# Performance work log

Hardware: AMD Instinct MI355X
Metric: run time of the kernel (lower is better)

Reference implementation:

```python
import jax, jax.numpy as jnp
import numpy as np

D = 1024  # model_dim; d_ff == model_dim in this module
EPS = 1e-6

def setup_inputs() -> dict:
    key = jax.random.key(0)
    ks = jax.random.split(key, 8)
    s = 1.0 / np.sqrt(D)
    sg = 1.0 / np.sqrt(2 * D)
    return {
        "x": jax.random.normal(ks[0], (8, 2048, D), dtype=jnp.float32),
        "w1": jax.random.uniform(ks[1], (D, D), jnp.float32, -s, s),
        "b1": jnp.zeros((D,), jnp.float32),
        "w2": jax.random.uniform(ks[2], (D, D), jnp.float32, -s, s),
        "b2": jnp.zeros((D,), jnp.float32),
        "ln_g": jnp.ones((D,), jnp.float32),
        "ln_b": jnp.zeros((D,), jnp.float32),
        "wg": jax.random.uniform(ks[3], (2 * D, 2 * D), jnp.float32, -sg, sg),
        "bg": jnp.zeros((2 * D,), jnp.float32),
    }

def _layernorm(x, g, b):
    mu = jnp.mean(x, axis=-1, keepdims=True)
    var = jnp.mean(jnp.square(x - mu), axis=-1, keepdims=True)
    return (x - mu) * jax.lax.rsqrt(var + EPS) * g + b

def reference(x, w1, b1, w2, b2, ln_g, ln_b, wg, bg):
    B, S, d = x.shape
    # cumulative average: tril-normalized mask matmul == prefix-sum / position
    denom = jnp.arange(1, S + 1, dtype=x.dtype)[:, None]  # [S,1]
    avg = jnp.cumsum(x, axis=1) / denom                    # [B,S,D]
    # PositionwiseFeedForward (dropout is identity at inference)
    inter = jax.nn.relu(_layernorm(avg, ln_g, ln_b) @ w1 + b1)
    avg_out = inter @ w2 + b2 + avg
    # gating
    gates = jnp.concatenate([x, avg_out], axis=-1) @ wg + bg  # [B,S,2D]
    in_g, fg_g = jnp.split(gates, 2, axis=-1)
    gated = jax.nn.sigmoid(in_g) * x + jax.nn.sigmoid(fg_g) * avg_out
    return gated, avg_out
```

## Files before the change

kernel.cpp:

```cpp
#include <hip/hip_runtime.h>

typedef unsigned short u16;
typedef __attribute__((ext_vector_type(8))) short short8;
typedef __attribute__((ext_vector_type(8))) unsigned short ushort8;
typedef __attribute__((ext_vector_type(4))) float f32x4;
typedef __attribute__((ext_vector_type(4))) unsigned short u16x4;

#define DEV static __device__ __forceinline__

DEV u16 f2bf(float f){
    unsigned u = __float_as_uint(f);
    u += 0x7fffu + ((u >> 16) & 1u);
    return (u16)(u >> 16);
}
DEV float bf2f(u16 h){ return __uint_as_float(((unsigned)h) << 16); }
DEV float sigm(float v){ return 1.f / (1.f + __expf(-v)); }

DEV f32x4 MF(short8 a, short8 b, f32x4 c){
    return __builtin_amdgcn_mfma_f32_16x16x32_bf16(a, b, c, 0, 0, 0);
}
DEV void gload16(const void* g, u16* l){
    __builtin_amdgcn_global_load_lds(
        (const __attribute__((address_space(1))) void*)g,
        (__attribute__((address_space(3))) void*)l, 16, 0, 0);
}
DEV void stage_half(const char* gp, size_t K2, u16* dst){
    gload16(gp, dst);
    gload16(gp + (K2 << 3), dst + 512);
}

#define SBAR()   asm volatile("s_barrier" ::: "memory")
#define WVM(n)   asm volatile("s_waitcnt vmcnt(" #n ")" ::: "memory")
#define WLG(n)   asm volatile("s_waitcnt lgkmcnt(" #n ")" ::: "memory")
#define SCB()    __builtin_amdgcn_sched_barrier(0)

constexpr int Bn = 8, Sn = 2048, Dn = 1024;
constexpr int CH = 128, NC = Sn / CH;
constexpr size_t NTOK = (size_t)Bn * Sn;

__global__ __launch_bounds__(256) void k_wcvt(const float* __restrict__ w,
                                              u16* __restrict__ wt,
                                              int Kd, int Nd)
{
    __shared__ float tile[32][33];
    int nbn = Nd / 32;
    int bk = blockIdx.x / nbn, bn = blockIdx.x % nbn;
    int lx = threadIdx.x & 31, ly = threadIdx.x >> 5;
    #pragma unroll
    for (int i = 0; i < 32; i += 8)
        tile[ly + i][lx] = w[(size_t)(bk * 32 + ly + i) * Nd + bn * 32 + lx];
    __syncthreads();
    #pragma unroll
    for (int i = 0; i < 32; i += 8)
        wt[(size_t)(bn * 32 + ly + i) * Kd + bk * 32 + lx] = f2bf(tile[lx][ly + i]);
}

__global__ __launch_bounds__(256) void k_psum(const float* __restrict__ x,
                                              float* __restrict__ part)
{
    int bx = blockIdx.x;
    int dblk = bx & 3; bx >>= 2;
    int c = bx & (NC - 1), b = bx >> 4;
    int d = dblk * 256 + threadIdx.x;
    const float* px = x + ((size_t)b * Sn + (size_t)c * CH) * Dn + d;
    float s = 0.f;
    #pragma unroll 4
    for (int i = 0; i < CH; i++) s += px[(size_t)i * Dn];
    part[((size_t)b * NC + c) * Dn + d] = s;
}

__global__ __launch_bounds__(256) void k_pscan(float* part)
{
    int g = blockIdx.x * 256 + threadIdx.x;
    int b = g >> 10, d = g & 1023;
    float run = 0.f;
    #pragma unroll
    for (int c = 0; c < NC; c++){
        size_t idx = ((size_t)b * NC + c) * Dn + d;
        float v = part[idx]; part[idx] = run; run += v;
    }
}

__global__ __launch_bounds__(256) void k_avg(const float* __restrict__ x,
                                             const float* __restrict__ part,
                                             u16* __restrict__ avg,
                                             u16* __restrict__ cat)
{
    int bx = blockIdx.x;
    int dblk = bx & 3; bx >>= 2;
    int c = bx & (NC - 1), b = bx >> 4;
    int d = dblk * 256 + threadIdx.x;
    const float* px = x   + ((size_t)b * Sn + (size_t)c * CH) * Dn + d;
    u16*         pa = avg + ((size_t)b * Sn + (size_t)c * CH) * Dn + d;
    u16*         pc = cat + ((size_t)b * Sn + (size_t)c * CH) * 2048 + d;
    float run = part[((size_t)b * NC + c) * Dn + d];
    for (int i = 0; i < CH; i++){
        float v = px[(size_t)i * Dn];
        run += v;
        int s = c * CH + i;
        pa[(size_t)i * Dn] = f2bf(run / (float)(s + 1));
        pc[(size_t)i * 2048] = f2bf(v);
    }
}

__global__ __launch_bounds__(256) void k_ln(const u16* __restrict__ avg,
                                            const float* __restrict__ g,
                                            const float* __restrict__ bta,
                                            u16* __restrict__ out)
{
    size_t row = blockIdx.x;
    int t = threadIdx.x;
    u16x4 hv = ((const u16x4*)(avg + row * Dn))[t];
    float4 v = { bf2f(hv[0]), bf2f(hv[1]), bf2f(hv[2]), bf2f(hv[3]) };
    float s = v.x + v.y + v.z + v.w;
    float q = v.x * v.x + v.y * v.y + v.z * v.z + v.w * v.w;
    #pragma unroll
    for (int o = 32; o > 0; o >>= 1){
        s += __shfl_down(s, o, 64);
        q += __shfl_down(q, o, 64);
    }
    __shared__ float rs[4], rq[4];
    __shared__ float smu, srstd;
    int wid = t >> 6, lane = t & 63;
    if (lane == 0){ rs[wid] = s; rq[wid] = q; }
    __syncthreads();
    if (t == 0){
        float S = rs[0] + rs[1] + rs[2] + rs[3];
        float Q = rq[0] + rq[1] + rq[2] + rq[3];
        float mu = S * (1.f / Dn);
        float var = Q * (1.f / Dn) - mu * mu;
        smu = mu; srstd = rsqrtf(var + 1e-6f);
    }
    __syncthreads();
    float mu = smu, rstd = srstd;
    int d0 = t * 4;
    float4 gg = ((const float4*)g)[t];
    float4 bb = ((const float4*)bta)[t];
    u16x4 o;
    o[0] = f2bf((v.x - mu) * rstd * gg.x + bb.x);
    o[1] = f2bf((v.y - mu) * rstd * gg.y + bb.y);
    o[2] = f2bf((v.z - mu) * rstd * gg.z + bb.z);
    o[3] = f2bf((v.w - mu) * rstd * gg.w + bb.w);
    *(u16x4*)(out + row * Dn + d0) = o;
}

template<int EPI>
__global__ __launch_bounds__(512, 2)
void k_gemm(const u16* __restrict__ A, const u16* __restrict__ Bt,
            const float* __restrict__ bias,
            float* __restrict__ of, u16* __restrict__ ob,
            const u16* __restrict__ resid,
            int M, int N, int K)
{
    __shared__ u16 smem[2][2][2][8192];

    int nbn = (EPI == 3) ? 8 : (N >> 8);
    int nwg = (M >> 8) * nbn;
    int bid = blockIdx.x;
    int swz = (bid & 7) * (nwg >> 3) + (bid >> 3);
    int bm = swz / nbn, bn = swz - bm * nbn;
    int m0 = bm << 8;
    int n0 = (EPI == 3) ? (bn << 7) : (bn << 8);

    int tid  = threadIdx.x;
    int wid  = tid >> 6, lane = tid & 63;
    int wm   = wid >> 2, wn = wid & 3;
    int fr   = lane & 15, q = lane >> 4;

    int srow = (wid << 4) + (lane >> 3);
    int cb   = ((lane & 7) << 4) ^ (((lane >> 3) & 7) << 4);
    size_t K2 = (size_t)K * 2;
    int b1base = (EPI == 3) ? (1024 + n0) : (n0 + 128);
    const char* gA0 = (const char*)A  + (size_t)(m0 + srow) * K2 + cb;
    const char* gA1 = (const char*)A  + (size_t)(m0 + 128 + srow) * K2 + cb;
    const char* gB0 = (const char*)Bt + (size_t)(n0 + srow) * K2 + cb;
    const char* gB1 = (const char*)Bt + (size_t)(b1base + srow) * K2 + cb;
    int w16 = wid << 10;

    int xorE = (lane & 7) << 3;
    int cbE0 = ((q << 3) ^ xorE);
    int cbE1 = cbE0 ^ 32;
    int aOff = (wm * 64 + fr) * 64;
    int bOff = (wn * 32 + fr) * 64;

    f32x4 acc[8][4] = {};
    short8 a0f[4][2], a1f[4][2], b0f[2][2], b1f[2][2];
    int NT = K >> 6;

#define ST_A0(t) stage_half(gA0 + (size_t)(t) * 128, K2, &smem[(t)&1][0][0][w16])
#define ST_A1(t) stage_half(gA1 + (size_t)(t) * 128, K2, &smem[(t)&1][0][1][w16])
#define ST_B0(t) stage_half(gB0 + (size_t)(t) * 128, K2, &smem[(t)&1][1][0][w16])
#define ST_B1(t) stage_half(gB1 + (size_t)(t) * 128, K2, &smem[(t)&1][1][1][w16])
#define RD_A(Fr, t, half) { const u16* _p = &smem[(t)&1][0][half][0];           \
    _Pragma("unroll") for (int i = 0; i < 4; i++){                              \
        Fr[i][0] = *(const short8*)&_p[aOff + i * 1024 + cbE0];                 \
        Fr[i][1] = *(const short8*)&_p[aOff + i * 1024 + cbE1]; } }
#define RD_B(Fr, t, half) { const u16* _p = &smem[(t)&1][1][half][0];           \
    _Pragma("unroll") for (int i = 0; i < 2; i++){                              \
        Fr[i][0] = *(const short8*)&_p[bOff + i * 1024 + cbE0];                 \
        Fr[i][1] = *(const short8*)&_p[bOff + i * 1024 + cbE1]; } }
#define MMQ(Af, Bf, mo, no)                                                     \
    __builtin_amdgcn_s_setprio(1);                                              \
    _Pragma("unroll") for (int mi = 0; mi < 4; mi++)                            \
        _Pragma("unroll") for (int ni = 0; ni < 2; ni++){                       \
            acc[mi+(mo)][ni+(no)] = MF(Af[mi][0], Bf[ni][0], acc[mi+(mo)][ni+(no)]); \
            acc[mi+(mo)][ni+(no)] = MF(Af[mi][1], Bf[ni][1], acc[mi+(mo)][ni+(no)]); \
        }                                                                        \
    __builtin_amdgcn_s_setprio(0);

    ST_A0(0); ST_B0(0); ST_B1(0); ST_A1(0); ST_A0(1); ST_B0(1); ST_B1(1);
    WVM(12); SBAR();
    RD_A(a0f, 0, 0);

    for (int t = 0; t + 2 < NT; ++t){
        WVM(8); SBAR();
        ST_A1(t + 1);
        RD_B(b0f, t, 0); SCB();
        RD_B(b1f, t, 1);
        WLG(4); SCB();
        MMQ(a0f, b0f, 0, 0);
        WVM(8); SBAR();
        ST_A0(t + 2);
        RD_A(a1f, t, 1);
        WLG(8); SCB();
        MMQ(a0f, b1f, 0, 2);
        SBAR();
        ST_B0(t + 2);
        WLG(0); SCB();
        MMQ(a1f, b1f, 4, 2);
        WVM(10); SBAR();
        ST_B1(t + 2);
        RD_A(a0f, t + 1, 0);
        WLG(8); SCB();
        MMQ(a1f, b0f, 4, 0);
    }
    {
        int t = NT - 2;
        WVM(8); SBAR();
        ST_A1(t + 1);
        RD_B(b0f, t, 0); SCB();
        RD_B(b1f, t, 1);
        WLG(4); SCB();
        MMQ(a0f, b0f, 0, 0);
        WVM(8); SBAR();
        RD_A(a1f, t, 1);
        WLG(8); SCB();
        MMQ(a0f, b1f, 0, 2);
        SBAR();
        WLG(0); SCB();
        MMQ(a1f, b1f, 4, 2);
        WVM(6); SBAR();
        RD_A(a0f, t + 1, 0);
        WLG(8); SCB();
        MMQ(a1f, b0f, 4, 0);
    }
    {
        int t = NT - 1;
        WVM(2); SBAR();
        RD_B(b0f, t, 0); SCB();
        RD_B(b1f, t, 1);
        WLG(4); SCB();
        MMQ(a0f, b0f, 0, 0);
        WVM(0); SBAR();
        RD_A(a1f, t, 1);
        WLG(8); SCB();
        MMQ(a0f, b1f, 0, 2);
        SBAR();
        WLG(0); SCB();
        MMQ(a1f, b1f, 4, 2);
        MMQ(a1f, b0f, 4, 0);
    }

    int col = lane & 15, rb = q * 4;

    if constexpr (EPI == 3){
        u16* s_in = &smem[0][0][0][0];
        u16* s_fg = s_in + 32768;
        float bi[2], bf_[2];
        #pragma unroll
        for (int ni = 0; ni < 2; ni++){
            bi[ni]  = bias[n0 + wn * 32 + ni * 16 + col];
            bf_[ni] = bias[1024 + n0 + wn * 32 + ni * 16 + col];
        }
        SBAR();
        #pragma unroll
        for (int mi = 0; mi < 8; mi++){
            int lrow = ((mi & 4) << 5) + wm * 64 + ((mi & 3) << 4) + rb;
            #pragma unroll
            for (int ni = 0; ni < 2; ni++){
                int c  = wn * 32 + ni * 16 + col;
                int cp = c ^ (q << 4);
                #pragma unroll
                for (int r = 0; r < 4; r++){
                    int row = lrow + r;
                    s_in[row * 128 + cp] = f2bf(sigm(acc[mi][ni][r] + bi[ni]));
                    s_fg[row * 128 + cp] = f2bf(sigm(acc[mi][ni + 2][r] + bf_[ni]));
                }
            }
        }
        WLG(0); SBAR();
        int rbase = wid * 32;
        #pragma unroll
        for (int rg = 0; rg < 8; rg++){
            int b4  = rbase + rg * 4;
            int row = b4 + (lane >> 4);
            int sw  = ((b4 >> 2) & 3) << 4;
            int c0  = (lane & 15) * 8;
            int cp  = c0 ^ sw;
            ushort8 iv = *(const ushort8*)&s_in[row * 128 + cp];
            ushort8 fv = *(const ushort8*)&s_fg[row * 128 + cp];
            size_t ga = (size_t)(m0 + row) * 2048 + n0 + c0;
            ushort8 xv = *(const ushort8*)&A[ga];
            ushort8 av = *(const ushort8*)&A[ga + 1024];
            size_t gb = (size_t)(m0 + row) * Dn + n0 + c0;
            float4 o0, o1;
            o0.x = bf2f(iv[0]) * bf2f(xv[0]) + bf2f(fv[0]) * bf2f(av[0]);
            o0.y = bf2f(iv[1]) * bf2f(xv[1]) + bf2f(fv[1]) * bf2f(av[1]);
            o0.z = bf2f(iv[2]) * bf2f(xv[2]) + bf2f(fv[2]) * bf2f(av[2]);
            o0.w = bf2f(iv[3]) * bf2f(xv[3]) + bf2f(fv[3]) * bf2f(av[3]);
            o1.x = bf2f(iv[4]) * bf2f(xv[4]) + bf2f(fv[4]) * bf2f(av[4]);
            o1.y = bf2f(iv[5]) * bf2f(xv[5]) + bf2f(fv[5]) * bf2f(av[5]);
            o1.z = bf2f(iv[6]) * bf2f(xv[6]) + bf2f(fv[6]) * bf2f(av[6]);
            o1.w = bf2f(iv[7]) * bf2f(xv[7]) + bf2f(fv[7]) * bf2f(av[7]);
            *(float4*)&of[gb] = o0;
            *(float4*)&of[gb + 4] = o1;
        }
        return;
    }

    #pragma unroll
    for (int mi = 0; mi < 8; mi++){
        int lrow = m0 + ((mi & 4) << 5) + wm * 64 + ((mi & 3) << 4) + rb;
        #pragma unroll
        for (int ni = 0; ni < 4; ni++){
            int gn = n0 + ((ni & 2) << 6) + wn * 32 + ((ni & 1) << 4) + col;
            float bv = bias[gn];
            #pragma unroll
            for (int r = 0; r < 4; r++){
                int gm = lrow + r;
                float v = acc[mi][ni][r] + bv;
                if constexpr (EPI == 1){
                    ob[(size_t)gm * N + gn] = f2bf(fmaxf(v, 0.f));
                } else {
                    v += bf2f(resid[(size_t)gm * N + gn]);
                    of[(size_t)gm * N + gn] = v;
                    ob[(size_t)gm * 2 * N + N + gn] = f2bf(v);
                }
            }
        }
    }
}

extern "C" void kernel_launch(void* const* d_in, const int* in_sizes, int n_in,
                              void* d_out, int out_size, void* d_ws, size_t ws_size,
                              hipStream_t stream)
{
    const float* x   = (const float*)d_in[0];
    const float* w1  = (const float*)d_in[1];
    const float* b1  = (const float*)d_in[2];
    const float* w2  = (const float*)d_in[3];
    const float* b2  = (const float*)d_in[4];
    const float* lng = (const float*)d_in[5];
    const float* lnb = (const float*)d_in[6];
    const float* wg  = (const float*)d_in[7];
    const float* bg  = (const float*)d_in[8];

    float* gated   = (float*)d_out;
    float* avg_out = (float*)d_out + NTOK * Dn;

    char* ws = (char*)d_ws;
    u16*   w1t   = (u16*)  (ws + (0ull   << 20));
    u16*   w2t   = (u16*)  (ws + (2ull   << 20));
    u16*   wgt   = (u16*)  (ws + (4ull   << 20));
    float* part  = (float*)(ws + (12ull  << 20));
    u16*   avg   = (u16*)  (ws + (16ull  << 20));
    u16*   ln    = (u16*)  (ws + (80ull  << 20));
    u16*   inter = (u16*)  (ws + (112ull << 20));
    u16*   cat   = (u16*)  (ws + (144ull << 20));

    k_wcvt<<<dim3(32 * 32), 256, 0, stream>>>(w1, w1t, Dn, Dn);
    k_wcvt<<<dim3(32 * 32), 256, 0, stream>>>(w2, w2t, Dn, Dn);
    k_wcvt<<<dim3(64 * 64), 256, 0, stream>>>(wg, wgt, 2 * Dn, 2 * Dn);

    k_psum <<<dim3(Bn * NC * 4), 256, 0, stream>>>(x, part);
    k_pscan<<<dim3(Bn * Dn / 256), 256, 0, stream>>>(part);
    k_avg  <<<dim3(Bn * NC * 4), 256, 0, stream>>>(x, part, avg, cat);

    k_ln<<<dim3((int)NTOK), 256, 0, stream>>>(avg, lng, lnb, ln);

    k_gemm<1><<<dim3((int)(NTOK / 256) * (Dn / 256)), 512, 0, stream>>>(
        ln, w1t, b1, nullptr, inter, nullptr, (int)NTOK, Dn, Dn);
    k_gemm<2><<<dim3((int)(NTOK / 256) * (Dn / 256)), 512, 0, stream>>>(
        inter, w2t, b2, avg_out, cat, avg, (int)NTOK, Dn, Dn);

    k_gemm<3><<<dim3((int)(NTOK / 256) * 8), 512, 0, stream>>>(
        cat, wgt, bg, gated, nullptr, nullptr, (int)NTOK, 2 * Dn, 2 * Dn);
}
```

Measured before the change: 302.3 us.

## Simplify GEMM main loop to one-tile lookahead with per-quadrant staging

Result: no change. 304.0 us (+0.6%).

```diff
diff --git a/kernel.cpp b/kernel.cpp
--- a/kernel.cpp
+++ b/kernel.cpp
@@ -201,74 +201,51 @@
         Fr[i][1] = *(const short8*)&_p[bOff + i * 1024 + cbE1]; } }
 #define MMQ(Af, Bf, mo, no)                                                     \
     __builtin_amdgcn_s_setprio(1);                                              \
-    _Pragma("unroll") for (int mi = 0; mi < 4; mi++)                            \
-        _Pragma("unroll") for (int ni = 0; ni < 2; ni++){                       \
-            acc[mi+(mo)][ni+(no)] = MF(Af[mi][0], Bf[ni][0], acc[mi+(mo)][ni+(no)]); \
-            acc[mi+(mo)][ni+(no)] = MF(Af[mi][1], Bf[ni][1], acc[mi+(mo)][ni+(no)]); \
-        }                                                                        \
+    _Pragma("unroll") for (int k = 0; k < 2; k++)                               \
+        _Pragma("unroll") for (int mi = 0; mi < 4; mi++)                        \
+            _Pragma("unroll") for (int ni = 0; ni < 2; ni++)                    \
+                acc[mi+(mo)][ni+(no)] = MF(Af[mi][k], Bf[ni][k],                \
+                                           acc[mi+(mo)][ni+(no)]);              \
     __builtin_amdgcn_s_setprio(0);
 
-    ST_A0(0); ST_B0(0); ST_B1(0); ST_A1(0); ST_A0(1); ST_B0(1); ST_B1(1);
-    WVM(12); SBAR();
-    RD_A(a0f, 0, 0);
-
-    for (int t = 0; t + 2 < NT; ++t){
-        WVM(8); SBAR();
+    ST_A0(0); ST_B0(0); ST_A1(0); ST_B1(0);
+
+    for (int t = 0; t + 1 < NT; ++t){
+        WVM(4); SBAR();
+        ST_A0(t + 1);
+        RD_A(a0f, t, 0);
+        RD_B(b0f, t, 0);
+        WLG(0); SCB();
+        MMQ(a0f, b0f, 0, 0);
+        WVM(4); SBAR();
+        ST_B0(t + 1);
+        RD_A(a1f, t, 1);
+        WLG(0); SCB();
+        MMQ(a1f, b0f, 4, 0);
+        WVM(4); SBAR();
         ST_A1(t + 1);
-        RD_B(b0f, t, 0); SCB();
         RD_B(b1f, t, 1);
-        WLG(4); SCB();
-        MMQ(a0f, b0f, 0, 0);
-        WVM(8); SBAR();
-        ST_A0(t + 2);
-        RD_A(a1f, t, 1);
-        WLG(8); SCB();
+        WLG(0); SCB();
+        MMQ(a1f, b1f, 4, 2);
+        ST_B1(t + 1);
         MMQ(a0f, b1f, 0, 2);
-        SBAR();
-        ST_B0(t + 2);
-        WLG(0); SCB();
-        MMQ(a1f, b1f, 4, 2);
-        WVM(10); SBAR();
-        ST_B1(t + 2);
-        RD_A(a0f, t + 1, 0);
-        WLG(8); SCB();
-        MMQ(a1f, b0f, 4, 0);
-    }
-    {
-        int t = NT - 2;
-        WVM(8); SBAR();
-        ST_A1(t + 1);
-        RD_B(b0f, t, 0); SCB();
-        RD_B(b1f, t, 1);
-        WLG(4); SCB();
-        MMQ(a0f, b0f, 0, 0);
-        WVM(8); SBAR();
-        RD_A(a1f, t, 1);
-        WLG(8); SCB();
-        MMQ(a0f, b1f, 0, 2);
-        SBAR();
-        WLG(0); SCB();
-        MMQ(a1f, b1f, 4, 2);
-        WVM(6); SBAR();
-        RD_A(a0f, t + 1, 0);
-        WLG(8); SCB();
-        MMQ(a1f, b0f, 4, 0);
     }
     {
         int t = NT - 1;
+        WVM(4); SBAR();
+        RD_A(a0f, t, 0);
+        RD_B(b0f, t, 0);
+        WLG(0); SCB();
+        MMQ(a0f, b0f, 0, 0);
         WVM(2); SBAR();
-        RD_B(b0f, t, 0); SCB();
+        RD_A(a1f, t, 1);
+        WLG(0); SCB();
+        MMQ(a1f, b0f, 4, 0);
+        WVM(0); SBAR();
         RD_B(b1f, t, 1);
-        WLG(4); SCB();
-        MMQ(a0f, b0f, 0, 0);
-        WVM(0); SBAR();
-        RD_A(a1f, t, 1);
-        WLG(8); SCB();
+        WLG(0); SCB();
+        MMQ(a1f, b1f, 4, 2);
         MMQ(a0f, b1f, 0, 2);
-        SBAR();
-        WLG(0); SCB();
-        MMQ(a1f, b1f, 4, 2);
-        MMQ(a1f, b0f, 4, 0);
     }
 
     int col = lane & 15, rb = q * 4;
```
